# Optimization experiments

Measured on AMD Instinct MI355X. Metric: run time of the kernel, lower is better.

The kernel has to match this reference:

```python
import jax, jax.numpy as jnp
import numpy as np

KERNEL_NUM = 21
SIGMA = 0.1
EXACT_SIGMA = 0.001
VOCAB, EMB_DIM = 50000, 128
B, LQ, LD = 1024, 64, 256
EPS = 1e-12  # torch F.normalize eps


def _kernel_params():
    # mus: midpoints of linspace(-1,1,21) via convolve with [0.5,0.5], trimmed -> 20 values
    mus = np.convolve(np.linspace(-1.0, 1.0, KERNEL_NUM), np.array([0.5, 0.5]))[1:-1]
    mus = np.concatenate([mus, np.array([1.0])])            # + exact-match kernel
    sigmas = np.concatenate([np.full(KERNEL_NUM - 1, SIGMA), np.array([EXACT_SIGMA])])
    return jnp.asarray(mus, jnp.float32), jnp.asarray(sigmas, jnp.float32)


def setup_inputs() -> dict:
    key = jax.random.key(0)
    ks = jax.random.split(key, 9)
    emb = jax.random.normal(ks[0], (VOCAB, EMB_DIM), jnp.float32)
    emb = emb.at[0].set(0.0)  # padding_idx=0 row is zero
    return {
        "query": jax.random.randint(ks[1], (B, LQ), 0, VOCAB),
        "document": jax.random.randint(ks[2], (B, LD), 0, VOCAB),
        "emb": emb,
        "W1": jax.random.normal(ks[3], (10, 21), jnp.float32) * 0.2,
        "b1": jax.random.normal(ks[4], (10,), jnp.float32) * 0.1,
        "W2": jax.random.normal(ks[5], (5, 10), jnp.float32) * 0.2,
        "b2": jax.random.normal(ks[6], (5,), jnp.float32) * 0.1,
        "W3": jax.random.normal(ks[7], (1, 5), jnp.float32) * 0.2,
        "b3": jax.random.normal(ks[8], (1,), jnp.float32) * 0.1,
    }


def _l2norm(x):
    n = jnp.linalg.norm(x, axis=-1, keepdims=True)
    return x / jnp.maximum(n, EPS)


def reference(query, document, emb, W1, b1, W2, b2, W3, b3):
    mus, sigmas = _kernel_params()
    q = _l2norm(emb[query])                       # [B, Lq, E]
    d = _l2norm(emb[document])                    # [B, Ld, E]
    mm = jnp.einsum("bqe,bde->bqd", q, d)         # cosine matching matrix [B, Lq, Ld]
    # all 21 Gaussian kernels in one pass: [B, Lq, Ld, K]
    diff = mm[..., None] - mus
    kvals = jnp.exp(-(diff * diff) / (2.0 * sigmas * sigmas))
    km = jnp.log1p(kvals.sum(axis=2)).sum(axis=1)  # sum over doc, log1p, sum over query -> [B, K]
    x = jax.nn.relu(km)
    x = jax.nn.relu(x @ W1.T + b1)
    x = x @ W2.T + b2
    return x @ W3.T + b3                           # [B, 1]
```

## Files before the change

kernel.cpp:

```cpp
#include <hip/hip_runtime.h>
#include <hip/hip_bf16.h>

#define L2E 1.4426950408889634f
#define LN2 0.6931471805599453f

#if defined(__has_builtin)
#if __has_builtin(__builtin_amdgcn_exp2f)
#define EXP2(x) __builtin_amdgcn_exp2f(x)
#else
#define EXP2(x) exp2f(x)
#endif
#if __has_builtin(__builtin_amdgcn_logf)
#define LOG2(x) __builtin_amdgcn_logf(x)
#else
#define LOG2(x) __log2f(x)
#endif
#else
#define EXP2(x) exp2f(x)
#define LOG2(x) __log2f(x)
#endif

typedef __attribute__((ext_vector_type(8))) short bf16x8;
typedef __attribute__((ext_vector_type(4))) float f32x4;
typedef __attribute__((ext_vector_type(2))) float f32x2;

__device__ __forceinline__ void gld_lds16(const void* g, void* l) {
  __builtin_amdgcn_global_load_lds(
      (const __attribute__((address_space(1))) void*)g,
      (__attribute__((address_space(3))) void*)l, 16, 0, 0);
}

__device__ __forceinline__ unsigned bf16rne(float f) {
  unsigned u = __float_as_uint(f);
  return (u + 0x7fffu + ((u >> 16) & 1u)) >> 16;
}

__global__ __launch_bounds__(256) void knrm_norm(const float* __restrict__ emb,
                                                 unsigned* __restrict__ embN) {
  const int t = threadIdx.x;
  const int l = t & 31;
  const int sub = (t >> 5) & 1;
  int wv = blockIdx.x * 4 + (t >> 6);
  const int nW = gridDim.x * 4;
  for (int rp = wv; rp < 25000; rp += nW) {
    int r = rp * 2 + sub;
    float4 v = *(const float4*)(emb + (size_t)r * 128 + l * 4);
    float ss = v.x * v.x + v.y * v.y + v.z * v.z + v.w * v.w;
#pragma unroll
    for (int m = 1; m < 32; m <<= 1) ss += __shfl_xor(ss, m, 64);
    float sc = 1.0f / fmaxf(sqrtf(ss), 1e-12f);
    uint2 o;
    o.x = bf16rne(v.x * sc) | (bf16rne(v.y * sc) << 16);
    o.y = bf16rne(v.z * sc) | (bf16rne(v.w * sc) << 16);
    *(uint2*)(embN + (size_t)r * 64 + l * 2) = o;
  }
}

__global__ __launch_bounds__(256, 4) void knrm_main(
    const int* __restrict__ query, const int* __restrict__ doc,
    const unsigned* __restrict__ embN,
    const float* __restrict__ W1, const float* __restrict__ b1,
    const float* __restrict__ W2, const float* __restrict__ b2,
    const float* __restrict__ W3, const float* __restrict__ b3,
    float* __restrict__ out) {
  __shared__ __align__(16) char dbuf[2][16 * 256];
  __shared__ float kmbuf[64 * 21];
  __shared__ int dtok[256];
  __shared__ float km2[4][21];
  __shared__ float kmv[21];
  __shared__ float x1[10];
  __shared__ float x2[5];

  const int b = blockIdx.x;
  const int tid = threadIdx.x;
  const int w = tid >> 6;
  const int lane = tid & 63;
  const int lo = lane & 15, hi = lane >> 4;
  const char* embB = (const char*)embN;

  dtok[tid] = doc[b * 256 + tid];

  const int myq = query[b * 64 + w * 16 + lo];
  bf16x8 bq[4];
#pragma unroll
  for (int kk = 0; kk < 4; ++kk)
    bq[kk] = *(const bf16x8*)(embB + (size_t)myq * 256 + kk * 64 + hi * 16);

  const int srow = tid >> 4;
  const int sslot = (tid & 15) ^ (srow & 7);
  {
    int tok = doc[b * 256 + srow];
    gld_lds16(embB + (size_t)tok * 256 + sslot * 16, dbuf[0] + w * 1024);
  }
  asm volatile("s_waitcnt vmcnt(0)" ::: "memory");
  __syncthreads();

  f32x2 acc20[20];
#pragma unroll
  for (int j = 0; j < 20; ++j) acc20[j] = (f32x2){0.0f, 0.0f};

#pragma unroll 1
  for (int s = 0; s < 16; ++s) {
    const int cur = s & 1;
    if (s < 15) {
      int tok = dtok[(s + 1) * 16 + srow];
      gld_lds16(embB + (size_t)tok * 256 + sslot * 16, dbuf[cur ^ 1] + w * 1024);
    }
    f32x4 mm = {0.0f, 0.0f, 0.0f, 0.0f};
#pragma unroll
    for (int kk = 0; kk < 4; ++kk) {
      int slot = (kk * 4 + hi) ^ (lo & 7);
      bf16x8 a = *(const bf16x8*)(dbuf[cur] + lo * 256 + slot * 16);
      mm = __builtin_amdgcn_mfma_f32_16x16x32_bf16(a, bq[kk], mm, 0, 0, 0);
    }
#pragma unroll
    for (int p = 0; p < 2; ++p) {
      f32x2 v = {mm[p], mm[p + 2]};
      f32x2 m = v * L2E;
      f32x2 a10 = m * 10.0f;
      f32x2 G, Gi, t9;
      G.x = EXP2(a10.x);
      G.y = EXP2(a10.y);
      Gi.x = EXP2(-a10.x);
      Gi.y = EXP2(-a10.y);
      f32x2 e9 = m * (v * -50.0f - 5.0f);
      t9.x = EXP2(e9.x);
      t9.y = EXP2(e9.y);
      f32x2 tu = t9, td = t9;
      acc20[9] += t9;
#pragma unroll
      for (int j = 10; j < 20; ++j) { tu *= G; acc20[j] += tu; }
#pragma unroll
      for (int j = 8; j >= 0; --j) { td *= Gi; acc20[j] += td; }
    }
    asm volatile("s_waitcnt vmcnt(0)" ::: "memory");
    __syncthreads();
  }

  int cnt = 0;
#pragma unroll 16
  for (int i = 0; i < 64; ++i) cnt += (dtok[hi * 64 + i] == myq) ? 1 : 0;
  cnt = (myq == 0) ? 0 : cnt;
  cnt += __shfl_xor(cnt, 16, 64);
  cnt += __shfl_xor(cnt, 32, 64);

  float sa[20];
#pragma unroll
  for (int j = 0; j < 20; ++j) {
    float s2 = acc20[j].x + acc20[j].y;
    s2 += __shfl_xor(s2, 16, 64);
    s2 += __shfl_xor(s2, 32, 64);
    sa[j] = s2;
  }

  if (hi == 0) {
    int q = w * 16 + lo;
#pragma unroll
    for (int j = 0; j < 20; ++j) kmbuf[q * 21 + j] = sa[j];
    kmbuf[q * 21 + 20] = (float)cnt;
  }
  __syncthreads();

  const float cA = -50.0f * L2E;
  if (tid < 84) {
    int j = tid % 21, c = tid / 21;
    float Cj = 1.0f;
    if (j < 20) {
      float mu = -0.95f + 0.1f * (float)j;
      Cj = EXP2(cA * mu * mu);
    }
    float s = 0.0f;
    for (int q = 0; q < 16; ++q)
      s += LOG2(fmaf(Cj, kmbuf[(c * 16 + q) * 21 + j], 1.0f));
    km2[c][j] = s * LN2;
  }
  __syncthreads();
  if (tid < 21)
    kmv[tid] = fmaxf(km2[0][tid] + km2[1][tid] + km2[2][tid] + km2[3][tid], 0.0f);
  __syncthreads();
  if (tid < 10) {
    float s = b1[tid];
    for (int j = 0; j < 21; ++j) s = fmaf(W1[tid * 21 + j], kmv[j], s);
    x1[tid] = fmaxf(s, 0.0f);
  }
  __syncthreads();
  if (tid < 5) {
    float s = b2[tid];
    for (int i = 0; i < 10; ++i) s = fmaf(W2[tid * 10 + i], x1[i], s);
    x2[tid] = s;
  }
  __syncthreads();
  if (tid == 0) {
    float s = b3[0];
    for (int i = 0; i < 5; ++i) s = fmaf(W3[i], x2[i], s);
    out[b] = s;
  }
}

extern "C" void kernel_launch(void* const* d_in, const int* in_sizes, int n_in,
                              void* d_out, int out_size, void* d_ws, size_t ws_size,
                              hipStream_t stream) {
  const int* query = (const int*)d_in[0];
  const int* doc = (const int*)d_in[1];
  const float* emb = (const float*)d_in[2];
  const float* W1 = (const float*)d_in[3];
  const float* b1 = (const float*)d_in[4];
  const float* W2 = (const float*)d_in[5];
  const float* b2 = (const float*)d_in[6];
  const float* W3 = (const float*)d_in[7];
  const float* b3 = (const float*)d_in[8];
  float* out = (float*)d_out;
  unsigned* embN = (unsigned*)d_ws;

  hipLaunchKernelGGL(knrm_norm, dim3(1024), dim3(256), 0, stream, emb, embN);
  hipLaunchKernelGGL(knrm_main, dim3(1024), dim3(256), 0, stream, query, doc, embN,
                     W1, b1, W2, b2, W3, b3, out);
}
```

Before: 41.12 us.

## Deepen doc-embedding prefetch to a 4-buffer ring and use packed FMA accumulation

Replaces the double-buffered LDS staging of document embeddings with a 4-slot ring that keeps three async global-to-LDS loads in flight, using graded vmcnt waits and raw s_barrier instead of a full drain plus __syncthreads each step. The kernel accumulation chain is rewritten with inline v_pk_fma_f32 and v_pk_mul_f32 so each accumulator update fuses the multiply and add on packed pairs. The aim is to hide gather latency better and cut VALU instruction count in the exp-heavy inner loop. In exchange it uses more LDS per block, which may reduce occupancy, and slightly changes rounding by fusing the multiply into the accumulate.

```diff
diff --git a/kernel.cpp b/kernel.cpp
--- a/kernel.cpp
+++ b/kernel.cpp
@@ -63,7 +63,7 @@
     const float* __restrict__ W2, const float* __restrict__ b2,
     const float* __restrict__ W3, const float* __restrict__ b3,
     float* __restrict__ out) {
-  __shared__ __align__(16) char dbuf[2][16 * 256];
+  __shared__ __align__(16) char dbuf[4][16 * 256];
   __shared__ float kmbuf[64 * 21];
   __shared__ int dtok[256];
   __shared__ float km2[4][21];
@@ -88,54 +88,66 @@
 
   const int srow = tid >> 4;
   const int sslot = (tid & 15) ^ (srow & 7);
-  {
-    int tok = doc[b * 256 + srow];
-    gld_lds16(embB + (size_t)tok * 256 + sslot * 16, dbuf[0] + w * 1024);
-  }
-  asm volatile("s_waitcnt vmcnt(0)" ::: "memory");
-  __syncthreads();
+
+#pragma unroll
+  for (int s = 0; s < 3; ++s) {
+    int tok = doc[b * 256 + s * 16 + srow];
+    gld_lds16(embB + (size_t)tok * 256 + sslot * 16, dbuf[s] + w * 1024);
+  }
+  asm volatile("s_waitcnt lgkmcnt(0)" ::: "memory");
+  __builtin_amdgcn_s_barrier();
 
   f32x2 acc20[20];
 #pragma unroll
   for (int j = 0; j < 20; ++j) acc20[j] = (f32x2){0.0f, 0.0f};
 
+#define STAGE(S, VM)                                                         \
+  {                                                                          \
+    asm volatile("s_waitcnt vmcnt(" #VM ")" ::: "memory");                   \
+    __builtin_amdgcn_s_barrier();                                            \
+    __builtin_amdgcn_sched_barrier(0);                                       \
+    if ((S) + 3 < 16) {                                                      \
+      int tok = dtok[((S) + 3) * 16 + srow];                                 \
+      gld_lds16(embB + (size_t)tok * 256 + sslot * 16,                       \
+                dbuf[((S) + 3) & 3] + w * 1024);                             \
+    }                                                                        \
+    const char* buf = dbuf[(S) & 3];                                         \
+    f32x4 mm = {0.0f, 0.0f, 0.0f, 0.0f};                                     \
+    _Pragma("unroll")                                                        \
+    for (int kk = 0; kk < 4; ++kk) {                                         \
+      int slot = (kk * 4 + hi) ^ (lo & 7);       \
+      bf16x8 a = *(const bf16x8*)(buf + lo * 256 + slot * 16);               \
+      mm = __builtin_amdgcn_mfma_f32_16x16x32_bf16(a, bq[kk], mm, 0, 0, 0);  \
+    }                                                                        \
+                            \
+    _Pragma("unroll")                                                        \
+    for (int p = 0; p < 2; ++p) {                                            \
+      float vx = mm[p], vy = mm[p + 2];                                      \
+      float a10x = vx * (10.0f * L2E), a10y = vy * (10.0f * L2E);            \
+      f32x2 G = {EXP2(a10x), EXP2(a10y)};                                    \
+      f32x2 Gi = {EXP2(-a10x), EXP2(-a10y)};                                 \
+      f32x2 tu = {EXP2((vx * L2E) * fmaf(-50.0f, vx, -5.0f)),                \
+                  EXP2((vy * L2E) * fmaf(-50.0f, vy, -5.0f))};               \
+      f32x2 td = tu;                                                         \
+      asm("v_pk_add_f32 %0, %0, %1" : "+v"(acc20[9]) : "v"(tu));             \
+      _Pragma("unroll")                                                      \
+      for (int j = 10; j < 20; ++j) {                                        \
+        asm("v_pk_fma_f32 %0, %1, %2, %0" : "+v"(acc20[j]) : "v"(tu), "v"(G)); \
+        if (j < 19) asm("v_pk_mul_f32 %0, %0, %1" : "+v"(tu) : "v"(G));      \
+      }                                                                      \
+      _Pragma("unroll")                                                      \
+      for (int j = 8; j >= 0; --j) {                                         \
+        asm("v_pk_fma_f32 %0, %1, %2, %0" : "+v"(acc20[j]) : "v"(td), "v"(Gi)); \
+        if (j > 0) asm("v_pk_mul_f32 %0, %0, %1" : "+v"(td) : "v"(Gi));      \
+      }                                                                      \
+    }                                                                        \
+  }
+
 #pragma unroll 1
-  for (int s = 0; s < 16; ++s) {
-    const int cur = s & 1;
-    if (s < 15) {
-      int tok = dtok[(s + 1) * 16 + srow];
-      gld_lds16(embB + (size_t)tok * 256 + sslot * 16, dbuf[cur ^ 1] + w * 1024);
-    }
-    f32x4 mm = {0.0f, 0.0f, 0.0f, 0.0f};
-#pragma unroll
-    for (int kk = 0; kk < 4; ++kk) {
-      int slot = (kk * 4 + hi) ^ (lo & 7);
-      bf16x8 a = *(const bf16x8*)(dbuf[cur] + lo * 256 + slot * 16);
-      mm = __builtin_amdgcn_mfma_f32_16x16x32_bf16(a, bq[kk], mm, 0, 0, 0);
-    }
-#pragma unroll
-    for (int p = 0; p < 2; ++p) {
-      f32x2 v = {mm[p], mm[p + 2]};
-      f32x2 m = v * L2E;
-      f32x2 a10 = m * 10.0f;
-      f32x2 G, Gi, t9;
-      G.x = EXP2(a10.x);
-      G.y = EXP2(a10.y);
-      Gi.x = EXP2(-a10.x);
-      Gi.y = EXP2(-a10.y);
-      f32x2 e9 = m * (v * -50.0f - 5.0f);
-      t9.x = EXP2(e9.x);
-      t9.y = EXP2(e9.y);
-      f32x2 tu = t9, td = t9;
-      acc20[9] += t9;
-#pragma unroll
-      for (int j = 10; j < 20; ++j) { tu *= G; acc20[j] += tu; }
-#pragma unroll
-      for (int j = 8; j >= 0; --j) { td *= Gi; acc20[j] += td; }
-    }
-    asm volatile("s_waitcnt vmcnt(0)" ::: "memory");
-    __syncthreads();
-  }
+  for (int s = 0; s < 14; ++s) STAGE(s, 2);
+  STAGE(14, 1);
+  STAGE(15, 0);
+#undef STAGE
 
   int cnt = 0;
 #pragma unroll 16
```

New measurement: 42.14 us. 1.02x slower.

## Give each wave a private triple-buffered LDS ring and drop per-stage block barriers

Applied to the files above, without the earlier changes.

Each wave now gathers the full 16-row document tile into its own three-slot LDS ring, prefetching two stages ahead, and waits only with vmcnt. This removes every per-stage __syncthreads from the main loop. The Gaussian kernel accumulation now uses inline packed FMA and multiply instructions, and the kmbuf array is dropped by reusing the ring for the per-query partial sums. In exchange, each wave issues four times the global gathers, which should mostly hit in L2, and LDS per block rises to about 48KB, which may cut how many blocks fit on a CU.

```diff
diff --git a/kernel.cpp b/kernel.cpp
--- a/kernel.cpp
+++ b/kernel.cpp
@@ -63,8 +63,7 @@
     const float* __restrict__ W2, const float* __restrict__ b2,
     const float* __restrict__ W3, const float* __restrict__ b3,
     float* __restrict__ out) {
-  __shared__ __align__(16) char dbuf[2][16 * 256];
-  __shared__ float kmbuf[64 * 21];
+  __shared__ __align__(16) char dbuf[4][3][16 * 256];
   __shared__ int dtok[256];
   __shared__ float km2[4][21];
   __shared__ float kmv[21];
@@ -77,8 +76,7 @@
   const int lane = tid & 63;
   const int lo = lane & 15, hi = lane >> 4;
   const char* embB = (const char*)embN;
-
-  dtok[tid] = doc[b * 256 + tid];
+  char* ring = dbuf[w][0];
 
   const int myq = query[b * 64 + w * 16 + lo];
   bf16x8 bq[4];
@@ -86,56 +84,79 @@
   for (int kk = 0; kk < 4; ++kk)
     bq[kk] = *(const bf16x8*)(embB + (size_t)myq * 256 + kk * 64 + hi * 16);
 
-  const int srow = tid >> 4;
-  const int sslot = (tid & 15) ^ (srow & 7);
-  {
-    int tok = doc[b * 256 + srow];
-    gld_lds16(embB + (size_t)tok * 256 + sslot * 16, dbuf[0] + w * 1024);
-  }
-  asm volatile("s_waitcnt vmcnt(0)" ::: "memory");
-  __syncthreads();
+  dtok[tid] = doc[b * 256 + tid];
+  __syncthreads();
+
+  const int grow = lane >> 4;
+  const int gslot0 = lane & 15;
+#pragma unroll
+  for (int s = 0; s < 2; ++s) {
+#pragma unroll
+    for (int g = 0; g < 4; ++g) {
+      int r = g * 4 + grow;
+      int tok = dtok[s * 16 + r];
+      gld_lds16(embB + (size_t)tok * 256 + (size_t)(gslot0 ^ (r & 7)) * 16,
+                ring + s * 4096 + g * 1024);
+    }
+  }
 
   f32x2 acc20[20];
 #pragma unroll
   for (int j = 0; j < 20; ++j) acc20[j] = (f32x2){0.0f, 0.0f};
 
+#define STAGE(s, SLOT, PSLOT, VMLIT)                                          \
+  {                                                                           \
+    asm volatile("s_waitcnt vmcnt(" #VMLIT ")" ::: "memory");                 \
+    if ((s) + 2 < 16) {                                                       \
+      _Pragma("unroll")                                                       \
+      for (int g = 0; g < 4; ++g) {                                           \
+        int r = g * 4 + grow;                                                 \
+        int tok = dtok[((s) + 2) * 16 + r];                                   \
+        gld_lds16(embB + (size_t)tok * 256 + (size_t)(gslot0 ^ (r & 7)) * 16, \
+                  ring + (PSLOT)*4096 + g * 1024);                            \
+      }                                                                       \
+    }                                                                         \
+    const char* buf = ring + (SLOT)*4096;                                     \
+    f32x4 mm = {0.0f, 0.0f, 0.0f, 0.0f};                                      \
+    _Pragma("unroll")                                                         \
+    for (int kk = 0; kk < 4; ++kk) {                                          \
+      int slot = (kk * 4 + hi) ^ (lo & 7);        \
+      bf16x8 a = *(const bf16x8*)(buf + lo * 256 + slot * 16);                \
+      mm = __builtin_amdgcn_mfma_f32_16x16x32_bf16(a, bq[kk], mm, 0, 0, 0);   \
+    }                                                                         \
+              \
+    _Pragma("unroll")                                                         \
+    for (int p = 0; p < 2; ++p) {                                             \
+      float vx = mm[p], vy = mm[p + 2];                                       \
+      float a10x = vx * (10.0f * L2E), a10y = vy * (10.0f * L2E);             \
+      f32x2 G = {EXP2(a10x), EXP2(a10y)};                                     \
+      f32x2 Gi = {EXP2(-a10x), EXP2(-a10y)};                                  \
+      f32x2 tu = {EXP2((vx * L2E) * fmaf(-50.0f, vx, -5.0f)),                 \
+                  EXP2((vy * L2E) * fmaf(-50.0f, vy, -5.0f))};                \
+      f32x2 td = tu;                                                          \
+      asm("v_pk_add_f32 %0, %0, %1" : "+v"(acc20[9]) : "v"(tu));              \
+      _Pragma("unroll")                                                       \
+      for (int j = 10; j < 20; ++j) {                                         \
+        asm("v_pk_fma_f32 %0, %1, %2, %0" : "+v"(acc20[j]) : "v"(tu), "v"(G)); \
+        if (j < 19) asm("v_pk_mul_f32 %0, %0, %1" : "+v"(tu) : "v"(G));       \
+      }                                                                       \
+      _Pragma("unroll")                                                       \
+      for (int j = 8; j >= 0; --j) {                                          \
+        asm("v_pk_fma_f32 %0, %1, %2, %0" : "+v"(acc20[j]) : "v"(td), "v"(Gi)); \
+        if (j > 0) asm("v_pk_mul_f32 %0, %0, %1" : "+v"(td) : "v"(Gi));       \
+      }                                                                       \
+    }                                                                         \
+  }
+
 #pragma unroll 1
-  for (int s = 0; s < 16; ++s) {
-    const int cur = s & 1;
-    if (s < 15) {
-      int tok = dtok[(s + 1) * 16 + srow];
-      gld_lds16(embB + (size_t)tok * 256 + sslot * 16, dbuf[cur ^ 1] + w * 1024);
-    }
-    f32x4 mm = {0.0f, 0.0f, 0.0f, 0.0f};
-#pragma unroll
-    for (int kk = 0; kk < 4; ++kk) {
-      int slot = (kk * 4 + hi) ^ (lo & 7);
-      bf16x8 a = *(const bf16x8*)(dbuf[cur] + lo * 256 + slot * 16);
-      mm = __builtin_amdgcn_mfma_f32_16x16x32_bf16(a, bq[kk], mm, 0, 0, 0);
-    }
-#pragma unroll
-    for (int p = 0; p < 2; ++p) {
-      f32x2 v = {mm[p], mm[p + 2]};
-      f32x2 m = v * L2E;
-      f32x2 a10 = m * 10.0f;
-      f32x2 G, Gi, t9;
-      G.x = EXP2(a10.x);
-      G.y = EXP2(a10.y);
-      Gi.x = EXP2(-a10.x);
-      Gi.y = EXP2(-a10.y);
-      f32x2 e9 = m * (v * -50.0f - 5.0f);
-      t9.x = EXP2(e9.x);
-      t9.y = EXP2(e9.y);
-      f32x2 tu = t9, td = t9;
-      acc20[9] += t9;
-#pragma unroll
-      for (int j = 10; j < 20; ++j) { tu *= G; acc20[j] += tu; }
-#pragma unroll
-      for (int j = 8; j >= 0; --j) { td *= Gi; acc20[j] += td; }
-    }
-    asm volatile("s_waitcnt vmcnt(0)" ::: "memory");
-    __syncthreads();
-  }
+  for (int s5 = 0; s5 < 5; ++s5) {
+    int s = s5 * 3;
+    STAGE(s, 0, 2, 4);
+    STAGE(s + 1, 1, 0, 4);
+    STAGE(s + 2, 2, 1, 4);
+  }
+  STAGE(15, 0, 2, 0);
+#undef STAGE
 
   int cnt = 0;
 #pragma unroll 16
@@ -153,11 +174,11 @@
     sa[j] = s2;
   }
 
+  float* kmq = (float*)ring;
   if (hi == 0) {
-    int q = w * 16 + lo;
-#pragma unroll
-    for (int j = 0; j < 20; ++j) kmbuf[q * 21 + j] = sa[j];
-    kmbuf[q * 21 + 20] = (float)cnt;
+#pragma unroll
+    for (int j = 0; j < 20; ++j) kmq[lo * 21 + j] = sa[j];
+    kmq[lo * 21 + 20] = (float)cnt;
   }
   __syncthreads();
 
@@ -170,8 +191,10 @@
       Cj = EXP2(cA * mu * mu);
     }
     float s = 0.0f;
-    for (int q = 0; q < 16; ++q)
-      s += LOG2(fmaf(Cj, kmbuf[(c * 16 + q) * 21 + j], 1.0f));
+    for (int q = 0; q < 16; ++q) {
+      float raw = ((const float*)dbuf[c])[q * 21 + j];
+      s += LOG2(fmaf(Cj, raw, 1.0f));
+    }
     km2[c][j] = s * LN2;
   }
   __syncthreads();
```

Result: slower. 42.89 us (+4.3%).
